# Optimization experiments

Measured on AMD Instinct MI355X. Metric: run time of the kernel, lower is better.

Reference implementation:

```python
import jax, jax.numpy as jnp
import numpy as np
import math

B, C, L_MIX, L_REF = 4, 512, 2048, 2048
NUM_HEADS = 8
HEAD_DIM = C // NUM_HEADS
MAX_LEN = 5000
EPS = 1e-5


def layer_norm(x, gamma, beta):
    mu = jnp.mean(x, axis=-1, keepdims=True)
    var = jnp.mean(jnp.square(x - mu), axis=-1, keepdims=True)
    return (x - mu) * jax.lax.rsqrt(var + EPS) * gamma + beta


def setup_inputs() -> dict:
    key = jax.random.key(0)
    ks = jax.random.split(key, 12)
    inp = {
        "query": jax.random.normal(ks[0], (B, C, L_MIX), dtype=jnp.float32),
        "key_value": jax.random.normal(ks[1], (B, C, L_REF), dtype=jnp.float32),
        "pos_encoding": jax.random.normal(ks[2], (1, MAX_LEN, C), dtype=jnp.float32) * 0.01,
        "q_gamma": jnp.ones((C,), jnp.float32),
        "q_beta": jnp.zeros((C,), jnp.float32),
        "k_gamma": jnp.ones((C,), jnp.float32),
        "k_beta": jnp.zeros((C,), jnp.float32),
        "Wq": jax.random.normal(ks[3], (C, C), jnp.float32) / math.sqrt(C),
        "bq": jax.random.normal(ks[4], (C,), jnp.float32) * 0.01,
        "Wk": jax.random.normal(ks[5], (C, C), jnp.float32) / math.sqrt(C),
        "bk": jax.random.normal(ks[6], (C,), jnp.float32) * 0.01,
        "Wv": jax.random.normal(ks[7], (C, C), jnp.float32) / math.sqrt(C),
        "bv": jax.random.normal(ks[8], (C,), jnp.float32) * 0.01,
        "Wo": jax.random.normal(ks[9], (C, C), jnp.float32) / math.sqrt(C),
        "bo": jax.random.normal(ks[10], (C,), jnp.float32) * 0.01,
    }
    return inp


def reference(query, key_value, pos_encoding, q_gamma, q_beta, k_gamma, k_beta,
              Wq, bq, Wk, bk, Wv, bv, Wo, bo):
    # (B, C, L) -> (B, L, C)
    q = jnp.transpose(query, (0, 2, 1))
    kv = jnp.transpose(key_value, (0, 2, 1))
    Lm, Lr = q.shape[1], kv.shape[1]
    q = q + pos_encoding[:, :Lm, :]
    kv = kv + pos_encoding[:, :Lr, :]
    q = layer_norm(q, q_gamma, q_beta)
    kv = layer_norm(kv, k_gamma, k_beta)
    Q = q @ Wq + bq          # (B, Lm, C)
    K = kv @ Wk + bk         # (B, Lr, C)
    V = kv @ Wv + bv         # (B, Lr, C)
    Q = Q.reshape(B, Lm, NUM_HEADS, HEAD_DIM)
    K = K.reshape(B, Lr, NUM_HEADS, HEAD_DIM)
    V = V.reshape(B, Lr, NUM_HEADS, HEAD_DIM)
    scale = math.sqrt(HEAD_DIM)
    scores = jnp.einsum('bqhd,bkhd->bhqk', Q, K) / scale  # (B, H, Lm, Lr)
    scores = jnp.clip(scores, -50.0, 50.0)
    attn = jax.nn.softmax(scores, axis=-1)  # dropout is identity at eval
    out = jnp.einsum('bhqk,bkhd->bqhd', attn, V).reshape(B, Lm, C)
    out = out @ Wo + bo
    out = out + q            # residual with normed/pos-encoded query, per source
    return jnp.transpose(out, (0, 2, 1))  # (B, C, Lm)
```

## Files before the change

### kernel.cpp

```cpp
#include <hip/hip_runtime.h>
#include <hip/hip_bf16.h>

#define B_ 4
#define C_ 512
#define L_ 2048
#define H_ 8
#define D_ 64
#define EPS_ 1e-5f

using short8 = __attribute__((ext_vector_type(8))) short;
using s4v    = __attribute__((ext_vector_type(4))) short;
using f32x4  = __attribute__((ext_vector_type(4))) float;

#if defined(__has_builtin)
#if __has_builtin(__builtin_amdgcn_exp2f)
#define EXP2(x) __builtin_amdgcn_exp2f(x)
#else
#define EXP2(x) exp2f(x)
#endif
#else
#define EXP2(x) exp2f(x)
#endif

#define GLOAD_LDS16(g, l)                                                     \
  __builtin_amdgcn_global_load_lds(                                           \
      (const __attribute__((address_space(1))) void*)(g),                     \
      (__attribute__((address_space(3))) void*)(l), 16, 0, 0)

static __device__ __forceinline__ short f2bf(float f) {
  __hip_bfloat16 h = __float2bfloat16(f);
  return __builtin_bit_cast(short, h);
}
static __device__ __forceinline__ float bf2f(short s) {
  return __bfloat162float(__builtin_bit_cast(__hip_bfloat16, s));
}

__global__ __launch_bounds__(256) void k_convert_w(
    const float* __restrict__ Wq, const float* __restrict__ Wk,
    const float* __restrict__ Wv, const float* __restrict__ Wo,
    short* __restrict__ Wt) {
  int m = blockIdx.x, k0 = blockIdx.y * 32, n0 = blockIdx.z * 32;
  const float* W = (m == 0) ? Wq : (m == 1) ? Wk : (m == 2) ? Wv : Wo;
  __shared__ float T[32][33];
  int t = threadIdx.x;
  {
    int kl = t >> 3, n4 = (t & 7) * 4;
    float4 v = *(const float4*)(W + (size_t)(k0 + kl) * C_ + n0 + n4);
    T[kl][n4] = v.x; T[kl][n4 + 1] = v.y; T[kl][n4 + 2] = v.z; T[kl][n4 + 3] = v.w;
  }
  __syncthreads();
  {
    int nl = t >> 3, k4 = (t & 7) * 4;
    s4v o;
#pragma unroll
    for (int j = 0; j < 4; ++j) o[j] = f2bf(T[k4 + j][nl]);
    *(s4v*)(Wt + (size_t)(m * C_ + n0 + nl) * C_ + k0 + k4) = o;
  }
}

__global__ __launch_bounds__(256) void k_prep(
    const float* __restrict__ query, const float* __restrict__ kv,
    const float* __restrict__ pos,
    const float* __restrict__ qg, const float* __restrict__ qb,
    const float* __restrict__ kg, const float* __restrict__ kb,
    short* __restrict__ qn, short* __restrict__ kvn) {
  int l0 = blockIdx.x * 16;
  int b  = blockIdx.y;
  int z  = blockIdx.z;
  const float* src = z ? kv : query;
  const float* g   = z ? kg : qg;
  const float* be  = z ? kb : qb;
  short* dst       = z ? kvn : qn;

  __shared__ float T[16][516];
  __shared__ float mu_s[16], rs_s[16];
  int t = threadIdx.x;

  for (int i = 0; i < 32; ++i) {
    int flat = i * 256 + t;
    int c = flat >> 4, ll = flat & 15;
    T[ll][c] = src[(size_t)(b * C_ + c) * L_ + l0 + ll];
  }
  __syncthreads();
  for (int i = 0; i < 32; ++i) {
    int flat = i * 256 + t;
    int ll = flat >> 9, c = flat & 511;
    T[ll][c] += pos[(size_t)(l0 + ll) * C_ + c];
  }
  __syncthreads();
  {
    int row = t >> 4, j = t & 15;
    float s1 = 0.f, s2 = 0.f;
    for (int c = j; c < C_; c += 16) { float v = T[row][c]; s1 += v; s2 += v * v; }
    for (int m = 1; m < 16; m <<= 1) {
      s1 += __shfl_xor(s1, m, 64);
      s2 += __shfl_xor(s2, m, 64);
    }
    if (j == 0) {
      float mu  = s1 * (1.0f / C_);
      float var = s2 * (1.0f / C_) - mu * mu;
      mu_s[row] = mu;
      rs_s[row] = rsqrtf(var + EPS_);
    }
  }
  __syncthreads();
  for (int i = 0; i < 32; ++i) {
    int flat = i * 256 + t;
    int ll = flat >> 9, c = flat & 511;
    float v = (T[ll][c] - mu_s[ll]) * rs_s[ll] * g[c] + be[c];
    dst[(size_t)(b * L_ + l0 + ll) * C_ + c] = f2bf(v);
  }
}

__global__ __launch_bounds__(256) void k_gemm_qkv(
    const short* __restrict__ qn, const short* __restrict__ kvn,
    const short* __restrict__ Wt,
    const float* __restrict__ bq, const float* __restrict__ bk, const float* __restrict__ bv,
    short* __restrict__ Qw, short* __restrict__ Kw, short* __restrict__ Vw) {
  int z = blockIdx.z;
  const short* X    = z ? kvn : qn;
  const short* W    = Wt + (size_t)z * C_ * C_;
  const float* bias = (z == 0) ? bq : (z == 1) ? bk : bv;
  short* Y          = (z == 0) ? Qw : (z == 1) ? Kw : Vw;
  float sc          = (z == 0) ? 0.18033688f : 1.0f;

  int m0 = blockIdx.x * 128, n0 = blockIdx.y * 128;
  __shared__ alignas(16) short As[128 * 32];
  __shared__ alignas(16) short Bs[128 * 32];
  int t = threadIdx.x, lane = t & 63, w = t >> 6;
  int wm = w & 1, wn = w >> 1;
  int quad = lane >> 4, c = lane & 15;

  const short* Ag = X + (size_t)(m0 + w * 32 + (lane >> 2)) * C_ + (lane & 3) * 8;
  const short* Bg = W + (size_t)(n0 + w * 32 + (lane >> 2)) * C_ + (lane & 3) * 8;

  f32x4 zero4 = {0.f, 0.f, 0.f, 0.f};
  f32x4 acc[4][4];
  for (int i = 0; i < 4; ++i) for (int j = 0; j < 4; ++j) acc[i][j] = zero4;

  for (int k0 = 0; k0 < C_; k0 += 32) {
    __syncthreads();
#pragma unroll
    for (int j = 0; j < 2; ++j) {
      GLOAD_LDS16(Ag + (size_t)j * 16 * C_ + k0, As + (w * 32 + j * 16) * 32);
      GLOAD_LDS16(Bg + (size_t)j * 16 * C_ + k0, Bs + (w * 32 + j * 16) * 32);
    }
    __syncthreads();
    short8 a[4], bf[4];
#pragma unroll
    for (int i = 0; i < 4; ++i)
      a[i]  = *(const short8*)(As + (wm * 64 + i * 16 + c) * 32 + quad * 8);
#pragma unroll
    for (int i = 0; i < 4; ++i)
      bf[i] = *(const short8*)(Bs + (wn * 64 + i * 16 + c) * 32 + quad * 8);
#pragma unroll
    for (int i = 0; i < 4; ++i)
#pragma unroll
      for (int j = 0; j < 4; ++j)
        acc[i][j] = __builtin_amdgcn_mfma_f32_16x16x32_bf16(a[i], bf[j], acc[i][j], 0, 0, 0);
  }

#pragma unroll
  for (int i = 0; i < 4; ++i)
#pragma unroll
    for (int j = 0; j < 4; ++j) {
      int colg = n0 + wn * 64 + j * 16 + c;
      float bia = bias[colg];
      s4v o;
#pragma unroll
      for (int r = 0; r < 4; ++r) o[r] = f2bf((acc[i][j][r] + bia) * sc);
      int rowg = m0 + wm * 64 + i * 16 + quad * 4;
#pragma unroll
      for (int r = 0; r < 4; ++r) Y[(size_t)(rowg + r) * C_ + colg] = o[r];
    }
}

__global__ __launch_bounds__(256) void k_transpose_v(
    const short* __restrict__ Vw, short* __restrict__ Vtg) {
  int l0 = blockIdx.x * 64, h = blockIdx.y, b = blockIdx.z;
  __shared__ alignas(16) short T[64 * 64];
  int t = threadIdx.x;
#pragma unroll
  for (int p = 0; p < 2; ++p) {
    int flat = p * 256 + t;
    int l = flat >> 3, cc = flat & 7;
    int sw = (l & 7) ^ ((l >> 3) & 7);
    *(short8*)(T + l * 64 + ((cc ^ sw) << 3)) =
        *(const short8*)(Vw + ((size_t)(b * L_ + l0 + l) * H_ + h) * D_ + (cc << 3));
  }
  __syncthreads();
#pragma unroll
  for (int p = 0; p < 2; ++p) {
    int flat = p * 256 + t;
    int d = flat >> 3, l8 = (flat & 7) * 8;
    int sw_hi = (l8 >> 3) & 7;
    short8 o;
#pragma unroll
    for (int j = 0; j < 8; ++j) {
      int pc = (d >> 3) ^ j ^ sw_hi;
      o[j] = T[(l8 + j) * 64 + (pc << 3) + (d & 7)];
    }
    *(short8*)(Vtg + ((size_t)(b * H_ + h) * D_ + d) * L_ + l0 + l8) = o;
  }
}

#define LDP 72
#define LDC 68
__global__ __launch_bounds__(256, 3) void k_attn(
    const short* __restrict__ Qw, const short* __restrict__ Kw,
    const short* __restrict__ Vtg, short* __restrict__ Ow) {
  int l0 = blockIdx.x * 64;
  int h  = blockIdx.y;
  int b  = blockIdx.z;
  __shared__ alignas(16) short Pw[4][2][16 * LDP];
  __shared__ alignas(16) float Cbuf[64 * LDC];
  __shared__ float Lbuf[64];
  int t = threadIdx.x, lane = t & 63, w = t >> 6;
  int qh = w & 1, ls = w >> 1;
  int quad = lane >> 4, c = lane & 15;

  short8 qa[2][2];
#pragma unroll
  for (int s = 0; s < 2; ++s) {
    const short* qp = Qw + ((size_t)(b * L_ + l0 + qh * 32 + s * 16 + c) * H_ + h) * D_ + quad * 8;
    qa[s][0] = *(const short8*)qp;
    qa[s][1] = *(const short8*)(qp + 32);
  }

  f32x4 zero4 = {0.f, 0.f, 0.f, 0.f};
  f32x4 acc[2][4];
#pragma unroll
  for (int s = 0; s < 2; ++s)
    for (int dt = 0; dt < 4; ++dt) acc[s][dt] = zero4;
  float lsum[2] = {0.f, 0.f};

  const short* Kb = Kw + ((size_t)(b * L_) * H_ + h) * D_;
  const short* Vb = Vtg + (size_t)(b * H_ + h) * D_ * L_;

  for (int lr0 = ls * 64; lr0 < L_; lr0 += 128) {
    short8 kf[4][2], vf[4][2];
#pragma unroll
    for (int T = 0; T < 4; ++T) {
      const short* kp = Kb + (size_t)(lr0 + T * 16 + c) * (H_ * D_) + quad * 8;
      kf[T][0] = *(const short8*)kp;
      kf[T][1] = *(const short8*)(kp + 32);
    }
#pragma unroll
    for (int dt = 0; dt < 4; ++dt) {
      const short* vp = Vb + (size_t)(dt * 16 + c) * L_ + lr0 + quad * 8;
      vf[dt][0] = *(const short8*)vp;
      vf[dt][1] = *(const short8*)(vp + 32);
    }

#pragma unroll
    for (int s = 0; s < 2; ++s) {
      f32x4 st[4] = {zero4, zero4, zero4, zero4};
#pragma unroll
      for (int T = 0; T < 4; ++T) {
        st[T] = __builtin_amdgcn_mfma_f32_16x16x32_bf16(kf[T][0], qa[s][0], st[T], 0, 0, 0);
        st[T] = __builtin_amdgcn_mfma_f32_16x16x32_bf16(kf[T][1], qa[s][1], st[T], 0, 0, 0);
      }
      short* pb = &Pw[w][s][0];
#pragma unroll
      for (int T = 0; T < 4; ++T) {
        s4v pk;
#pragma unroll
        for (int r = 0; r < 4; ++r) {
          float p = EXP2(st[T][r]);
          lsum[s] += p;
          pk[r] = f2bf(p);
        }
        *(s4v*)(pb + c * LDP + T * 16 + quad * 4) = pk;
      }
#pragma unroll
      for (int hf = 0; hf < 2; ++hf) {
        short8 pf = *(const short8*)(pb + c * LDP + hf * 32 + quad * 8);
#pragma unroll
        for (int dt = 0; dt < 4; ++dt)
          acc[s][dt] = __builtin_amdgcn_mfma_f32_16x16x32_bf16(vf[dt][hf], pf, acc[s][dt], 0, 0, 0);
      }
    }
  }

#pragma unroll
  for (int s = 0; s < 2; ++s) {
    lsum[s] += __shfl_xor(lsum[s], 16, 64);
    lsum[s] += __shfl_xor(lsum[s], 32, 64);
  }

  if (ls == 1) {
#pragma unroll
    for (int s = 0; s < 2; ++s) {
      int q = qh * 32 + s * 16 + c;
#pragma unroll
      for (int dt = 0; dt < 4; ++dt)
        *(f32x4*)(Cbuf + q * LDC + dt * 16 + quad * 4) = acc[s][dt];
      if (quad == 0) Lbuf[q] = lsum[s];
    }
  }
  __syncthreads();
  if (ls == 0) {
#pragma unroll
    for (int s = 0; s < 2; ++s) {
      int q = qh * 32 + s * 16 + c;
      float inv = 1.0f / (lsum[s] + Lbuf[q]);
#pragma unroll
      for (int dt = 0; dt < 4; ++dt) {
        f32x4 o = *(const f32x4*)(Cbuf + q * LDC + dt * 16 + quad * 4);
        s4v ov;
#pragma unroll
        for (int r = 0; r < 4; ++r) ov[r] = f2bf((acc[s][dt][r] + o[r]) * inv);
        *(s4v*)(Ow + ((size_t)(b * L_ + l0 + q) * H_ + h) * D_ + dt * 16 + quad * 4) = ov;
      }
    }
  }
}

__global__ __launch_bounds__(256) void k_gemm_out(
    const short* __restrict__ Ow, const short* __restrict__ Wot,
    const float* __restrict__ bo, const short* __restrict__ qn,
    float* __restrict__ out) {
  int m0 = blockIdx.x * 128, n0 = blockIdx.y * 128;
  __shared__ alignas(16) short As[128 * 32];
  __shared__ alignas(16) short Bs[128 * 32];
  int t = threadIdx.x, lane = t & 63, w = t >> 6;
  int wm = w & 1, wn = w >> 1;
  int quad = lane >> 4, c = lane & 15;

  const short* Ag = Ow  + (size_t)(m0 + w * 32 + (lane >> 2)) * C_ + (lane & 3) * 8;
  const short* Bg = Wot + (size_t)(n0 + w * 32 + (lane >> 2)) * C_ + (lane & 3) * 8;

  f32x4 zero4 = {0.f, 0.f, 0.f, 0.f};
  f32x4 acc[4][4];
  for (int i = 0; i < 4; ++i) for (int j = 0; j < 4; ++j) acc[i][j] = zero4;

  for (int k0 = 0; k0 < C_; k0 += 32) {
    __syncthreads();
#pragma unroll
    for (int j = 0; j < 2; ++j) {
      GLOAD_LDS16(Ag + (size_t)j * 16 * C_ + k0, As + (w * 32 + j * 16) * 32);
      GLOAD_LDS16(Bg + (size_t)j * 16 * C_ + k0, Bs + (w * 32 + j * 16) * 32);
    }
    __syncthreads();
    short8 a[4], bf[4];
#pragma unroll
    for (int i = 0; i < 4; ++i)
      a[i]  = *(const short8*)(As + (wm * 64 + i * 16 + c) * 32 + quad * 8);
#pragma unroll
    for (int i = 0; i < 4; ++i)
      bf[i] = *(const short8*)(Bs + (wn * 64 + i * 16 + c) * 32 + quad * 8);
#pragma unroll
    for (int i = 0; i < 4; ++i)
#pragma unroll
      for (int j = 0; j < 4; ++j)
        acc[i][j] = __builtin_amdgcn_mfma_f32_16x16x32_bf16(a[i], bf[j], acc[i][j], 0, 0, 0);
  }

  int bb = m0 >> 11;
#pragma unroll
  for (int i = 0; i < 4; ++i)
#pragma unroll
    for (int j = 0; j < 4; ++j) {
      int colg = n0 + wn * 64 + j * 16 + c;
      float bia = bo[colg];
      int rowg = m0 + wm * 64 + i * 16 + quad * 4;
      int l = rowg & (L_ - 1);
      float4 vv;
      float* pv = &vv.x;
#pragma unroll
      for (int r = 0; r < 4; ++r)
        pv[r] = acc[i][j][r] + bia + bf2f(qn[(size_t)(rowg + r) * C_ + colg]);
      *(float4*)(out + ((size_t)bb * C_ + colg) * L_ + l) = vv;
    }
}

extern "C" void kernel_launch(void* const* d_in, const int* in_sizes, int n_in,
                              void* d_out, int out_size, void* d_ws, size_t ws_size,
                              hipStream_t stream) {
  const float* query     = (const float*)d_in[0];
  const float* key_value = (const float*)d_in[1];
  const float* pos       = (const float*)d_in[2];
  const float* qg        = (const float*)d_in[3];
  const float* qb        = (const float*)d_in[4];
  const float* kg        = (const float*)d_in[5];
  const float* kb        = (const float*)d_in[6];
  const float* Wq        = (const float*)d_in[7];
  const float* bq        = (const float*)d_in[8];
  const float* Wk        = (const float*)d_in[9];
  const float* bk        = (const float*)d_in[10];
  const float* Wv        = (const float*)d_in[11];
  const float* bv        = (const float*)d_in[12];
  const float* Wo        = (const float*)d_in[13];
  const float* bo        = (const float*)d_in[14];
  float* out = (float*)d_out;

  char* ws = (char*)d_ws;
  const size_t SZ = (size_t)B_ * L_ * C_ * 2;
  short* qn  = (short*)(ws + 0 * SZ);
  short* kvn = (short*)(ws + 1 * SZ);
  short* Qw  = (short*)(ws + 2 * SZ);
  short* Kw  = (short*)(ws + 3 * SZ);
  short* Vw  = (short*)(ws + 4 * SZ);
  short* Ow  = (short*)(ws + 5 * SZ);
  short* Wt  = (short*)(ws + 6 * SZ);
  short* Vtg = kvn;

  k_convert_w<<<dim3(4, 16, 16), 256, 0, stream>>>(Wq, Wk, Wv, Wo, Wt);
  k_prep<<<dim3(L_ / 16, B_, 2), 256, 0, stream>>>(query, key_value, pos, qg, qb, kg, kb, qn, kvn);
  k_gemm_qkv<<<dim3(8192 / 128, C_ / 128, 3), 256, 0, stream>>>(qn, kvn, Wt, bq, bk, bv, Qw, Kw, Vw);
  k_transpose_v<<<dim3(L_ / 64, H_, B_), 256, 0, stream>>>(Vw, Vtg);
  k_attn<<<dim3(L_ / 64, H_, B_), 256, 0, stream>>>(Qw, Kw, Vtg, Ow);
  k_gemm_out<<<dim3(8192 / 128, C_ / 128, 1), 256, 0, stream>>>(Ow, Wt + (size_t)3 * C_ * C_, bo, qn, out);
}
```

Baseline: 281.0 us.

## Vectorize prep, fuse V transpose into QKV GEMM, retile attention with K prefetch

The layernorm prep kernel now moves data with float4 loads and 4-wide bf16 stores instead of scalar accesses. The QKV GEMM epilogue writes V directly in transposed per-head layout, which removes the separate transpose kernel and one pass over V. The attention kernel now handles 128 queries per block, so each K/V fragment is reused across twice as many queries. It also double-buffers the K fragment registers to prefetch the next chunk, uses a 1D grid ordered batch-head first, and lowers the occupancy hint from 3 to 2 to fit the larger register footprint.

Measured after the change: 280.1 us. About the same (-0.3%).

```diff
diff --git a/kernel.cpp b/kernel.cpp
--- a/kernel.cpp
+++ b/kernel.cpp
@@ -72,20 +72,27 @@
   const float* be  = z ? kb : qb;
   short* dst       = z ? kvn : qn;
 
-  __shared__ float T[16][516];
+  __shared__ alignas(16) float T[16][516];
   __shared__ float mu_s[16], rs_s[16];
   int t = threadIdx.x;
 
-  for (int i = 0; i < 32; ++i) {
-    int flat = i * 256 + t;
-    int c = flat >> 4, ll = flat & 15;
-    T[ll][c] = src[(size_t)(b * C_ + c) * L_ + l0 + ll];
+#pragma unroll
+  for (int i = 0; i < 8; ++i) {
+    int idx = i * 256 + t;
+    int cc = idx >> 2, lg = (idx & 3) * 4;
+    float4 v = *(const float4*)(src + (size_t)(b * C_ + cc) * L_ + l0 + lg);
+    T[lg + 0][cc] = v.x; T[lg + 1][cc] = v.y; T[lg + 2][cc] = v.z; T[lg + 3][cc] = v.w;
   }
   __syncthreads();
-  for (int i = 0; i < 32; ++i) {
-    int flat = i * 256 + t;
-    int ll = flat >> 9, c = flat & 511;
-    T[ll][c] += pos[(size_t)(l0 + ll) * C_ + c];
+#pragma unroll
+  for (int i = 0; i < 8; ++i) {
+    int idx = i * 256 + t;
+    int ll = idx >> 7, c4 = (idx & 127) * 4;
+    float4 p = *(const float4*)(pos + (size_t)(l0 + ll) * C_ + c4);
+    float4* tp = (float4*)&T[ll][c4];
+    float4 cur = *tp;
+    cur.x += p.x; cur.y += p.y; cur.z += p.z; cur.w += p.w;
+    *tp = cur;
   }
   __syncthreads();
   {
@@ -104,11 +111,20 @@
     }
   }
   __syncthreads();
-  for (int i = 0; i < 32; ++i) {
-    int flat = i * 256 + t;
-    int ll = flat >> 9, c = flat & 511;
-    float v = (T[ll][c] - mu_s[ll]) * rs_s[ll] * g[c] + be[c];
-    dst[(size_t)(b * L_ + l0 + ll) * C_ + c] = f2bf(v);
+#pragma unroll
+  for (int i = 0; i < 8; ++i) {
+    int idx = i * 256 + t;
+    int ll = idx >> 7, c4 = (idx & 127) * 4;
+    float4 v  = *(const float4*)&T[ll][c4];
+    float4 gv = *(const float4*)(g + c4);
+    float4 bv = *(const float4*)(be + c4);
+    float mu = mu_s[ll], rs = rs_s[ll];
+    s4v o;
+    o[0] = f2bf((v.x - mu) * rs * gv.x + bv.x);
+    o[1] = f2bf((v.y - mu) * rs * gv.y + bv.y);
+    o[2] = f2bf((v.z - mu) * rs * gv.z + bv.z);
+    o[3] = f2bf((v.w - mu) * rs * gv.w + bv.w);
+    *(s4v*)(dst + (size_t)(b * L_ + l0 + ll) * C_ + c4) = o;
   }
 }
 
@@ -116,12 +132,11 @@
     const short* __restrict__ qn, const short* __restrict__ kvn,
     const short* __restrict__ Wt,
     const float* __restrict__ bq, const float* __restrict__ bk, const float* __restrict__ bv,
-    short* __restrict__ Qw, short* __restrict__ Kw, short* __restrict__ Vw) {
+    short* __restrict__ Qw, short* __restrict__ Kw, short* __restrict__ Vtg) {
   int z = blockIdx.z;
   const short* X    = z ? kvn : qn;
   const short* W    = Wt + (size_t)z * C_ * C_;
   const float* bias = (z == 0) ? bq : (z == 1) ? bk : bv;
-  short* Y          = (z == 0) ? Qw : (z == 1) ? Kw : Vw;
   float sc          = (z == 0) ? 0.18033688f : 1.0f;
 
   int m0 = blockIdx.x * 128, n0 = blockIdx.y * 128;
@@ -160,107 +175,98 @@
         acc[i][j] = __builtin_amdgcn_mfma_f32_16x16x32_bf16(a[i], bf[j], acc[i][j], 0, 0, 0);
   }
 
-#pragma unroll
-  for (int i = 0; i < 4; ++i)
-#pragma unroll
-    for (int j = 0; j < 4; ++j) {
-      int colg = n0 + wn * 64 + j * 16 + c;
-      float bia = bias[colg];
-      s4v o;
-#pragma unroll
-      for (int r = 0; r < 4; ++r) o[r] = f2bf((acc[i][j][r] + bia) * sc);
-      int rowg = m0 + wm * 64 + i * 16 + quad * 4;
-#pragma unroll
-      for (int r = 0; r < 4; ++r) Y[(size_t)(rowg + r) * C_ + colg] = o[r];
-    }
-}
-
-__global__ __launch_bounds__(256) void k_transpose_v(
-    const short* __restrict__ Vw, short* __restrict__ Vtg) {
-  int l0 = blockIdx.x * 64, h = blockIdx.y, b = blockIdx.z;
-  __shared__ alignas(16) short T[64 * 64];
-  int t = threadIdx.x;
-#pragma unroll
-  for (int p = 0; p < 2; ++p) {
-    int flat = p * 256 + t;
-    int l = flat >> 3, cc = flat & 7;
-    int sw = (l & 7) ^ ((l >> 3) & 7);
-    *(short8*)(T + l * 64 + ((cc ^ sw) << 3)) =
-        *(const short8*)(Vw + ((size_t)(b * L_ + l0 + l) * H_ + h) * D_ + (cc << 3));
-  }
-  __syncthreads();
-#pragma unroll
-  for (int p = 0; p < 2; ++p) {
-    int flat = p * 256 + t;
-    int d = flat >> 3, l8 = (flat & 7) * 8;
-    int sw_hi = (l8 >> 3) & 7;
-    short8 o;
-#pragma unroll
-    for (int j = 0; j < 8; ++j) {
-      int pc = (d >> 3) ^ j ^ sw_hi;
-      o[j] = T[(l8 + j) * 64 + (pc << 3) + (d & 7)];
-    }
-    *(short8*)(Vtg + ((size_t)(b * H_ + h) * D_ + d) * L_ + l0 + l8) = o;
+  if (z == 2) {
+#pragma unroll
+    for (int i = 0; i < 4; ++i)
+#pragma unroll
+      for (int j = 0; j < 4; ++j) {
+        int colg = n0 + wn * 64 + j * 16 + c;
+        float bia = bias[colg];
+        int hh = colg >> 6, dd = colg & 63;
+        int rowg = m0 + wm * 64 + i * 16 + quad * 4;
+        int bb = rowg >> 11, l = rowg & (L_ - 1);
+        s4v o;
+#pragma unroll
+        for (int r = 0; r < 4; ++r) o[r] = f2bf(acc[i][j][r] + bia);
+        *(s4v*)(Vtg + ((size_t)(bb * H_ + hh) * D_ + dd) * L_ + l) = o;
+      }
+  } else {
+    short* Y = (z == 0) ? Qw : Kw;
+#pragma unroll
+    for (int i = 0; i < 4; ++i)
+#pragma unroll
+      for (int j = 0; j < 4; ++j) {
+        int colg = n0 + wn * 64 + j * 16 + c;
+        float bia = bias[colg];
+        int rowg = m0 + wm * 64 + i * 16 + quad * 4;
+#pragma unroll
+        for (int r = 0; r < 4; ++r)
+          Y[(size_t)(rowg + r) * C_ + colg] = f2bf((acc[i][j][r] + bia) * sc);
+      }
   }
 }
 
 #define LDP 72
 #define LDC 68
-__global__ __launch_bounds__(256, 3) void k_attn(
+__global__ __launch_bounds__(256, 2) void k_attn(
     const short* __restrict__ Qw, const short* __restrict__ Kw,
     const short* __restrict__ Vtg, short* __restrict__ Ow) {
-  int l0 = blockIdx.x * 64;
-  int h  = blockIdx.y;
-  int b  = blockIdx.z;
-  __shared__ alignas(16) short Pw[4][2][16 * LDP];
-  __shared__ alignas(16) float Cbuf[64 * LDC];
-  __shared__ float Lbuf[64];
+  int bh = blockIdx.x & 31;
+  int l0 = (blockIdx.x >> 5) * 128;
+  int b = bh >> 3, h = bh & 7;
+  __shared__ alignas(16) short Pw[4][16 * LDP];
+  __shared__ alignas(16) float Cbuf[128 * LDC];
+  __shared__ float Lbuf[128];
   int t = threadIdx.x, lane = t & 63, w = t >> 6;
   int qh = w & 1, ls = w >> 1;
   int quad = lane >> 4, c = lane & 15;
 
-  short8 qa[2][2];
-#pragma unroll
-  for (int s = 0; s < 2; ++s) {
-    const short* qp = Qw + ((size_t)(b * L_ + l0 + qh * 32 + s * 16 + c) * H_ + h) * D_ + quad * 8;
+  short8 qa[4][2];
+#pragma unroll
+  for (int s = 0; s < 4; ++s) {
+    const short* qp = Qw + ((size_t)(b * L_ + l0 + qh * 64 + s * 16 + c) * H_ + h) * D_ + quad * 8;
     qa[s][0] = *(const short8*)qp;
     qa[s][1] = *(const short8*)(qp + 32);
   }
 
   f32x4 zero4 = {0.f, 0.f, 0.f, 0.f};
-  f32x4 acc[2][4];
-#pragma unroll
-  for (int s = 0; s < 2; ++s)
+  f32x4 acc[4][4];
+#pragma unroll
+  for (int s = 0; s < 4; ++s)
     for (int dt = 0; dt < 4; ++dt) acc[s][dt] = zero4;
-  float lsum[2] = {0.f, 0.f};
+  float lsum[4] = {0.f, 0.f, 0.f, 0.f};
 
   const short* Kb = Kw + ((size_t)(b * L_) * H_ + h) * D_;
   const short* Vb = Vtg + (size_t)(b * H_ + h) * D_ * L_;
-
-  for (int lr0 = ls * 64; lr0 < L_; lr0 += 128) {
-    short8 kf[4][2], vf[4][2];
+  short* pb = &Pw[w][0];
+
+  short8 kf[2][4][2];
+  auto loadK = [&](int buf, int lr) {
 #pragma unroll
     for (int T = 0; T < 4; ++T) {
-      const short* kp = Kb + (size_t)(lr0 + T * 16 + c) * (H_ * D_) + quad * 8;
-      kf[T][0] = *(const short8*)kp;
-      kf[T][1] = *(const short8*)(kp + 32);
-    }
+      const short* kp = Kb + (size_t)(lr + T * 16 + c) * C_ + quad * 8;
+      kf[buf][T][0] = *(const short8*)kp;
+      kf[buf][T][1] = *(const short8*)(kp + 32);
+    }
+  };
+
+  auto chunk = [&](int buf, int lr0, int lrn) {
+    loadK(buf ^ 1, lrn);
+    short8 vf[4][2];
 #pragma unroll
     for (int dt = 0; dt < 4; ++dt) {
       const short* vp = Vb + (size_t)(dt * 16 + c) * L_ + lr0 + quad * 8;
       vf[dt][0] = *(const short8*)vp;
       vf[dt][1] = *(const short8*)(vp + 32);
     }
-
-#pragma unroll
-    for (int s = 0; s < 2; ++s) {
+#pragma unroll
+    for (int s = 0; s < 4; ++s) {
       f32x4 st[4] = {zero4, zero4, zero4, zero4};
 #pragma unroll
       for (int T = 0; T < 4; ++T) {
-        st[T] = __builtin_amdgcn_mfma_f32_16x16x32_bf16(kf[T][0], qa[s][0], st[T], 0, 0, 0);
-        st[T] = __builtin_amdgcn_mfma_f32_16x16x32_bf16(kf[T][1], qa[s][1], st[T], 0, 0, 0);
-      }
-      short* pb = &Pw[w][s][0];
+        st[T] = __builtin_amdgcn_mfma_f32_16x16x32_bf16(kf[buf][T][0], qa[s][0], st[T], 0, 0, 0);
+        st[T] = __builtin_amdgcn_mfma_f32_16x16x32_bf16(kf[buf][T][1], qa[s][1], st[T], 0, 0, 0);
+      }
 #pragma unroll
       for (int T = 0; T < 4; ++T) {
         s4v pk;
@@ -280,18 +286,25 @@
           acc[s][dt] = __builtin_amdgcn_mfma_f32_16x16x32_bf16(vf[dt][hf], pf, acc[s][dt], 0, 0, 0);
       }
     }
-  }
-
-#pragma unroll
-  for (int s = 0; s < 2; ++s) {
+  };
+
+  loadK(0, ls * 64);
+  for (int i = 0; i < 8; ++i) {
+    int lr0 = ls * 64 + i * 256;
+    chunk(0, lr0, lr0 + 128);
+    chunk(1, lr0 + 128, (i == 7) ? ls * 64 : lr0 + 256);
+  }
+
+#pragma unroll
+  for (int s = 0; s < 4; ++s) {
     lsum[s] += __shfl_xor(lsum[s], 16, 64);
     lsum[s] += __shfl_xor(lsum[s], 32, 64);
   }
 
   if (ls == 1) {
 #pragma unroll
-    for (int s = 0; s < 2; ++s) {
-      int q = qh * 32 + s * 16 + c;
+    for (int s = 0; s < 4; ++s) {
+      int q = qh * 64 + s * 16 + c;
 #pragma unroll
       for (int dt = 0; dt < 4; ++dt)
         *(f32x4*)(Cbuf + q * LDC + dt * 16 + quad * 4) = acc[s][dt];
@@ -301,8 +314,8 @@
   __syncthreads();
   if (ls == 0) {
 #pragma unroll
-    for (int s = 0; s < 2; ++s) {
-      int q = qh * 32 + s * 16 + c;
+    for (int s = 0; s < 4; ++s) {
+      int q = qh * 64 + s * 16 + c;
       float inv = 1.0f / (lsum[s] + Lbuf[q]);
 #pragma unroll
       for (int dt = 0; dt < 4; ++dt) {
@@ -400,15 +413,13 @@
   short* kvn = (short*)(ws + 1 * SZ);
   short* Qw  = (short*)(ws + 2 * SZ);
   short* Kw  = (short*)(ws + 3 * SZ);
-  short* Vw  = (short*)(ws + 4 * SZ);
+  short* Vtg = (short*)(ws + 4 * SZ);
   short* Ow  = (short*)(ws + 5 * SZ);
   short* Wt  = (short*)(ws + 6 * SZ);
-  short* Vtg = kvn;
 
   k_convert_w<<<dim3(4, 16, 16), 256, 0, stream>>>(Wq, Wk, Wv, Wo, Wt);
   k_prep<<<dim3(L_ / 16, B_, 2), 256, 0, stream>>>(query, key_value, pos, qg, qb, kg, kb, qn, kvn);
-  k_gemm_qkv<<<dim3(8192 / 128, C_ / 128, 3), 256, 0, stream>>>(qn, kvn, Wt, bq, bk, bv, Qw, Kw, Vw);
-  k_transpose_v<<<dim3(L_ / 64, H_, B_), 256, 0, stream>>>(Vw, Vtg);
-  k_attn<<<dim3(L_ / 64, H_, B_), 256, 0, stream>>>(Qw, Kw, Vtg, Ow);
+  k_gemm_qkv<<<dim3(8192 / 128, C_ / 128, 3), 256, 0, stream>>>(qn, kvn, Wt, bq, bk, bv, Qw, Kw, Vtg);
+  k_attn<<<dim3(512), 256, 0, stream>>>(Qw, Kw, Vtg, Ow);
   k_gemm_out<<<dim3(8192 / 128, C_ / 128, 1), 256, 0, stream>>>(Ow, Wt + (size_t)3 * C_ * C_, bo, qn, out);
 }
```
